# Optimization experiments

Measured on AMD Instinct MI355X. Metric: run time of the kernel, lower is better.

The kernel has to match this reference:

```python
import jax, jax.numpy as jnp
import numpy as np

S = 512      # seq_len -> S*S - S edges
V = 32000    # vocab_size
D = 128      # d_model
H = 4        # num_heads
L = 2        # num_layers
DN = 64      # d_node
DE = 64      # d_edge
DF = 4 * D   # ffn hidden
TEMP = 1.0   # temperature_init
E = S * S - S


def setup_inputs() -> dict:
    key = jax.random.key(0)
    ks = jax.random.split(key, 12)
    n = lambda k, shp: jax.random.normal(k, shp, dtype=jnp.float32) * 0.02
    return {
        "token_ids": jax.random.randint(ks[0], (S,), 0, V),
        "u": jax.random.uniform(ks[1], (E,), dtype=jnp.float32),
        "emb": n(ks[2], (V, D)),
        "Wqkv": n(ks[3], (L, D, 3 * D)), "bqkv": jnp.zeros((L, 3 * D)),
        "Wo": n(ks[4], (L, D, D)), "bo": jnp.zeros((L, D)),
        "ln1_g": jnp.ones((L, D)), "ln1_b": jnp.zeros((L, D)),
        "Wff1": n(ks[5], (L, D, DF)), "bff1": jnp.zeros((L, DF)),
        "Wff2": n(ks[6], (L, DF, D)), "bff2": jnp.zeros((L, D)),
        "ln2_g": jnp.ones((L, D)), "ln2_b": jnp.zeros((L, D)),
        "node_W": n(ks[7], (D, DN)), "node_b": jnp.zeros((DN,)),
        "sc_W1": n(ks[8], (2 * D + 1, D)), "sc_b1": jnp.zeros((D,)),
        "sc_W2": n(ks[9], (D, 1)), "sc_b2": jnp.zeros((1,)),
        "te_W": n(ks[10], (2 * D + 1, DE)), "te_b": jnp.zeros((DE,)),
    }


def _layernorm(x, g, b):
    m = jnp.mean(x, -1, keepdims=True)
    v = jnp.var(x, -1, keepdims=True)
    return (x - m) * jax.lax.rsqrt(v + 1e-5) * g + b


def _pos_encoding(s, d):
    pos = jnp.arange(s, dtype=jnp.float32)[:, None]
    div = jnp.exp(jnp.arange(0, d, 2, dtype=jnp.float32) * (-np.log(10000.0) / d))
    pe = jnp.zeros((s, d), dtype=jnp.float32)
    pe = pe.at[:, 0::2].set(jnp.sin(pos * div)).at[:, 1::2].set(jnp.cos(pos * div))
    return pe


_SRC_NP = np.repeat(np.arange(S), S)
_TGT_NP = np.tile(np.arange(S), S)
_KEEP = _SRC_NP != _TGT_NP
SRC = jnp.asarray(_SRC_NP[_KEEP])  # [E] static off-diagonal indices
TGT = jnp.asarray(_TGT_NP[_KEEP])


def _forward(token_ids, u, emb, Wqkv, bqkv, Wo, bo, ln1_g, ln1_b, Wff1, bff1,
             Wff2, bff2, ln2_g, ln2_b, node_W, node_b, sc_W1, sc_b1, sc_W2,
             sc_b2, te_W, te_b):
    # --- mini transformer backbone ---
    x = emb[token_ids] + _pos_encoding(S, D)  # [S, D]
    dh = D // H
    for l in range(L):
        qkv = x @ Wqkv[l] + bqkv[l]
        q, k, v = jnp.split(qkv, 3, axis=-1)
        q = q.reshape(S, H, dh); k = k.reshape(S, H, dh); v = v.reshape(S, H, dh)
        scores = jnp.einsum('qhd,khd->hqk', q, k) / np.sqrt(dh).astype(np.float32)
        attn = jax.nn.softmax(scores, axis=-1)
        o = jnp.einsum('hqk,khd->qhd', attn, v).reshape(S, D)
        x = _layernorm(x + o @ Wo[l] + bo[l], ln1_g[l], ln1_b[l])
        h = jax.nn.gelu(x @ Wff1[l] + bff1[l], approximate=False)
        x = _layernorm(x + h @ Wff2[l] + bff2[l], ln2_g[l], ln2_b[l])
    node_features = x @ node_W + node_b  # [S, DN]
    # --- all-pairs edge construction (off-diagonal) ---
    pos_diff = ((SRC - TGT).astype(jnp.float32) / S)[:, None]  # [E, 1]
    pair = jnp.concatenate([x[SRC], x[TGT], pos_diff], axis=-1)  # [E, 2D+1]
    # edge scorer MLP
    hs = jax.nn.gelu(pair @ sc_W1 + sc_b1, approximate=False)
    edge_logits = (hs @ sc_W2 + sc_b2)[:, 0]  # [E]
    # gumbel-sigmoid (soft, hard=False)
    uu = jnp.clip(u, 1e-8, 1.0 - 1e-8)
    gnoise = -jnp.log(-jnp.log(uu))
    edge_gates = jax.nn.sigmoid((edge_logits + gnoise) / TEMP)  # [E]
    # gated edge features
    edge_feats = (pair @ te_W + te_b) * edge_gates[:, None]  # [E, DE]
    return node_features, edge_feats, edge_gates


def reference(token_ids, u, emb, Wqkv, bqkv, Wo, bo, ln1_g, ln1_b, Wff1, bff1,
              Wff2, bff2, ln2_g, ln2_b, node_W, node_b, sc_W1, sc_b1, sc_W2,
              sc_b2, te_W, te_b):
    node_features, edge_feats, edge_gates = _forward(
        token_ids, u, emb, Wqkv, bqkv, Wo, bo, ln1_g, ln1_b, Wff1, bff1,
        Wff2, bff2, ln2_g, ln2_b, node_W, node_b, sc_W1, sc_b1, sc_W2,
        sc_b2, te_W, te_b)
    edge_index = jnp.stack([SRC, TGT])  # [2, E]
    return node_features, edge_feats, edge_index, edge_gates
```

## Files before the change

kernel.cpp:

```cpp
#include <hip/hip_runtime.h>
#include <math.h>

#define SS 512
#define DD 128
#define HH 4
#define DHH 32
#define DFF 512
#define E_EDGES 261632

__device__ __forceinline__ float gelu_f(float v) {
    return 0.5f * v * (1.0f + erff(v * 0.70710678118654752f));
}
__device__ __forceinline__ float fgelu(float x) {
    float x2 = x * x;
    float z = x * fmaf(0.044715f, x2, 1.0f) * -1.5957691216057308f;
    float e = __expf(z);
    return x * __builtin_amdgcn_rcpf(1.0f + e);
}

__global__ __launch_bounds__(128) void k_embed(const int* __restrict__ tok,
                                               const float* __restrict__ emb,
                                               float* __restrict__ x) {
    int s = blockIdx.x;
    int d = threadIdx.x;
    float v = emb[(size_t)tok[s] * DD + d];
    int i2 = (d >> 1) << 1;
    float div = expf(-(float)i2 * (9.210340371976184f / 128.0f));
    float arg = (float)s * div;
    v += (d & 1) ? cosf(arg) : sinf(arg);
    x[s * DD + d] = v;
}

__global__ __launch_bounds__(384) void k_qkv(const float* __restrict__ x,
                                             const float* __restrict__ W,
                                             const float* __restrict__ b,
                                             float* __restrict__ qkv) {
    __shared__ float xs[4][DD];
    int r0 = blockIdx.x * 4;
    int c = threadIdx.x;
    for (int i = threadIdx.x; i < 4 * DD; i += 384)
        xs[i >> 7][i & 127] = x[(r0 + (i >> 7)) * DD + (i & 127)];
    __syncthreads();
    float a0 = 0, a1 = 0, a2 = 0, a3 = 0;
    for (int d = 0; d < DD; ++d) {
        float w = W[d * 384 + c];
        a0 += xs[0][d] * w; a1 += xs[1][d] * w;
        a2 += xs[2][d] * w; a3 += xs[3][d] * w;
    }
    float bb = b[c];
    qkv[(r0 + 0) * 384 + c] = a0 + bb;
    qkv[(r0 + 1) * 384 + c] = a1 + bb;
    qkv[(r0 + 2) * 384 + c] = a2 + bb;
    qkv[(r0 + 3) * 384 + c] = a3 + bb;
}

__global__ __launch_bounds__(256) void k_attn(const float* __restrict__ qkv,
                                              float* __restrict__ o) {
    int qi = blockIdx.x;
    int tid = threadIdx.x;
    int h = tid >> 6, lane = tid & 63;
    __shared__ float sq[DD];
    __shared__ float ps[HH][SS];
    __shared__ float tile[64 * 129];
    if (tid < DD) sq[tid] = qkv[qi * 384 + tid];
    const float scale = 0.17677669529663687f;
    float sc[8];
    float m = -1e30f;
    for (int kk = 0; kk < 8; ++kk) {
        __syncthreads();
        for (int i = tid * 4; i < 64 * 128; i += 1024) {
            int r = i >> 7, c = i & 127;
            const float4 v = *reinterpret_cast<const float4*>(&qkv[(kk * 64 + r) * 384 + 128 + c]);
            tile[r * 129 + c + 0] = v.x;
            tile[r * 129 + c + 1] = v.y;
            tile[r * 129 + c + 2] = v.z;
            tile[r * 129 + c + 3] = v.w;
        }
        __syncthreads();
        float acc = 0.f;
        #pragma unroll
        for (int d = 0; d < DHH; ++d)
            acc += sq[h * DHH + d] * tile[lane * 129 + h * DHH + d];
        acc *= scale;
        sc[kk] = acc;
        m = fmaxf(m, acc);
    }
    for (int off = 32; off; off >>= 1) m = fmaxf(m, __shfl_xor(m, off));
    float sum = 0.f;
    for (int kk = 0; kk < 8; ++kk) { sc[kk] = __expf(sc[kk] - m); sum += sc[kk]; }
    for (int off = 32; off; off >>= 1) sum += __shfl_xor(sum, off);
    float inv = 1.0f / sum;
    for (int kk = 0; kk < 8; ++kk) ps[h][kk * 64 + lane] = sc[kk] * inv;
    __syncthreads();
    int d = lane & 31, hh2 = lane >> 5;
    float acc = 0.f;
    for (int i = 0; i < 256; ++i) {
        int ki = hh2 * 256 + i;
        acc += ps[h][ki] * qkv[ki * 384 + 256 + h * DHH + d];
    }
    acc += __shfl_down(acc, 32);
    if (lane < 32) o[qi * DD + h * DHH + d] = acc;
}

__global__ __launch_bounds__(256) void k_tail(const float* __restrict__ o,
                                              const float* __restrict__ Wo,
                                              const float* __restrict__ bo,
                                              const float* __restrict__ g1,
                                              const float* __restrict__ b1,
                                              const float* __restrict__ W1,
                                              const float* __restrict__ bf1,
                                              const float* __restrict__ W2,
                                              const float* __restrict__ bf2,
                                              const float* __restrict__ g2,
                                              const float* __restrict__ b2,
                                              float* __restrict__ x) {
    int r0 = blockIdx.x * 2;
    int tid = threadIdx.x;
    int grp = tid >> 7, c = tid & 127;
    int wig = (tid >> 6) & 1;
    __shared__ float osr[2][DD];
    __shared__ float x1[2][DD];
    __shared__ float hh[2][DFF];
    __shared__ float red[2][2];
    osr[grp][c] = o[(r0 + grp) * DD + c];
    float xres = x[(r0 + grp) * DD + c];
    __syncthreads();
    float acc = 0.f;
    for (int d = 0; d < DD; ++d) acc += osr[grp][d] * Wo[d * DD + c];
    float val = xres + acc + bo[c];
    float sum = val;
    for (int off = 32; off; off >>= 1) sum += __shfl_xor(sum, off);
    if ((tid & 63) == 0) red[grp][wig] = sum;
    __syncthreads();
    float mean = (red[grp][0] + red[grp][1]) * (1.0f / 128.0f);
    float dv = val - mean;
    float sq = dv * dv;
    for (int off = 32; off; off >>= 1) sq += __shfl_xor(sq, off);
    __syncthreads();
    if ((tid & 63) == 0) red[grp][wig] = sq;
    __syncthreads();
    float var = (red[grp][0] + red[grp][1]) * (1.0f / 128.0f);
    float xv = dv * rsqrtf(var + 1e-5f) * g1[c] + b1[c];
    x1[grp][c] = xv;
    __syncthreads();
    {
        int c0 = tid, c1 = tid + 256;
        float s00 = 0, s01 = 0, s10 = 0, s11 = 0;
        for (int d = 0; d < DD; ++d) {
            float xa = x1[0][d], xb = x1[1][d];
            float w0 = W1[d * DFF + c0], w1 = W1[d * DFF + c1];
            s00 = fmaf(xa, w0, s00); s10 = fmaf(xb, w0, s10);
            s01 = fmaf(xa, w1, s01); s11 = fmaf(xb, w1, s11);
        }
        hh[0][c0] = gelu_f(s00 + bf1[c0]);
        hh[1][c0] = gelu_f(s10 + bf1[c0]);
        hh[0][c1] = gelu_f(s01 + bf1[c1]);
        hh[1][c1] = gelu_f(s11 + bf1[c1]);
    }
    __syncthreads();
    float acc2 = 0.f;
    for (int d = 0; d < DFF; ++d) acc2 += hh[grp][d] * W2[d * DD + c];
    float val2 = x1[grp][c] + acc2 + bf2[c];
    float sum2 = val2;
    for (int off = 32; off; off >>= 1) sum2 += __shfl_xor(sum2, off);
    if ((tid & 63) == 0) red[grp][wig] = sum2;
    __syncthreads();
    float mean2 = (red[grp][0] + red[grp][1]) * (1.0f / 128.0f);
    float dv2 = val2 - mean2;
    float sq2 = dv2 * dv2;
    for (int off = 32; off; off >>= 1) sq2 += __shfl_xor(sq2, off);
    __syncthreads();
    if ((tid & 63) == 0) red[grp][wig] = sq2;
    __syncthreads();
    float var2 = (red[grp][0] + red[grp][1]) * (1.0f / 128.0f);
    x[(r0 + grp) * DD + c] = dv2 * rsqrtf(var2 + 1e-5f) * g2[c] + b2[c];
}

__global__ __launch_bounds__(448) void k_node_pre(const float* __restrict__ x,
                                                  const float* __restrict__ nodeW,
                                                  const float* __restrict__ nodeb,
                                                  const float* __restrict__ scW1,
                                                  const float* __restrict__ scb1,
                                                  const float* __restrict__ teW,
                                                  const float* __restrict__ teb,
                                                  float* __restrict__ out_node,
                                                  float* __restrict__ As,
                                                  float* __restrict__ At2,
                                                  float* __restrict__ Bs,
                                                  float* __restrict__ Bt) {
    __shared__ float xs[4][DD];
    int r0 = blockIdx.x * 4;
    for (int i = threadIdx.x; i < 4 * DD; i += 448)
        xs[i >> 7][i & 127] = x[(r0 + (i >> 7)) * DD + (i & 127)];
    __syncthreads();
    int c = threadIdx.x;
    const float* wp;
    int ldw;
    if (c < 64)       { wp = nodeW + c;                    ldw = 64;  }
    else if (c < 192) { wp = scW1 + (c - 64);              ldw = 128; }
    else if (c < 320) { wp = scW1 + 128 * 128 + (c - 192); ldw = 128; }
    else if (c < 384) { wp = teW + (c - 320);              ldw = 64;  }
    else              { wp = teW + 128 * 64 + (c - 384);   ldw = 64;  }
    float a[4] = {0, 0, 0, 0};
    for (int d = 0; d < DD; ++d) {
        float w = wp[d * ldw];
        a[0] += xs[0][d] * w; a[1] += xs[1][d] * w;
        a[2] += xs[2][d] * w; a[3] += xs[3][d] * w;
    }
    #pragma unroll
    for (int r = 0; r < 4; ++r) {
        int row = r0 + r;
        float v = a[r];
        if (c < 64)       out_node[row * 64 + c] = v + nodeb[c];
        else if (c < 192) As[row * 128 + (c - 64)] = v + scb1[c - 64];
        else if (c < 320) {
            int j = c - 192;
            At2[row * 128 + ((j & 63) * 2 + (j >> 6))] = v;
        }
        else if (c < 384) Bs[row * 64 + (c - 320)] = v + teb[c - 320];
        else              Bt[row * 64 + (c - 384)] = v;
    }
}

__global__ __launch_bounds__(256) void k_estatic(const float* __restrict__ u,
                                                 float* __restrict__ nl,
                                                 float* __restrict__ out_ei) {
    int e = blockIdx.x * 256 + threadIdx.x;
    if (e >= E_EDGES) return;
    int s = e / 511;
    int idx = e - s * 511;
    int t = idx + (idx >= s);
    out_ei[e] = (float)s;
    out_ei[E_EDGES + e] = (float)t;
    float uu = fminf(fmaxf(u[e], 1e-8f), 1.0f - 1e-8f);
    nl[e] = -__logf(uu);
}

__global__ __launch_bounds__(256) void k_edges(const float* __restrict__ As,
                                               const float* __restrict__ At2,
                                               const float* __restrict__ Bs,
                                               const float* __restrict__ Bt,
                                               const float* __restrict__ scW1,
                                               const float* __restrict__ scW2,
                                               const float* __restrict__ scb2p,
                                               const float* __restrict__ teW,
                                               const float* __restrict__ nl,
                                               float* __restrict__ out_feat,
                                               float* __restrict__ out_gate) {
    int s = blockIdx.x;
    int seg = blockIdx.y;
    __shared__ float lAs[128], lap[128], lw2[128], lBs[64], lbp[64];
    int tid = threadIdx.x;
    if (tid < 128) {
        lAs[tid] = As[s * 128 + tid];
        lap[tid] = scW1[256 * 128 + tid];
        lw2[tid] = scW2[tid];
    } else if (tid < 192) {
        int j = tid - 128;
        lBs[j] = Bs[s * 64 + j];
        lbp[j] = teW[256 * 64 + j];
    }
    __syncthreads();
    float scb2 = scb2p[0];
    int w = tid >> 6, lane = tid & 63;
    int j = lane;
    float cAs0 = lAs[j], cAs1 = lAs[j + 64];
    float cap0 = lap[j], cap1 = lap[j + 64];
    float cw0 = lw2[j], cw1 = lw2[j + 64];
    float cBs = lBs[j], cbp = lbp[j];
    for (int iter = 0; iter < 16; ++iter) {
        int idx = seg * 64 + iter * 4 + w;
        if (idx >= 511) continue;
        int t = idx + (idx >= s);
        int e = s * 511 + idx;
        float pd = (float)(s - t) * (1.0f / 512.0f);
        float2 at = *reinterpret_cast<const float2*>(&At2[(size_t)t * 128 + 2 * j]);
        float a0 = cAs0 + at.x + pd * cap0;
        float a1 = cAs1 + at.y + pd * cap1;
        float part = fgelu(a0) * cw0 + fgelu(a1) * cw1;
        for (int off = 32; off; off >>= 1) part += __shfl_xor(part, off);
        float logit = part + scb2;
        float gate = __builtin_amdgcn_rcpf(1.0f + nl[e] * __expf(-logit));
        float f = (cBs + Bt[t * 64 + j] + pd * cbp) * gate;
        out_feat[(size_t)e * 64 + j] = f;
        if (lane == 0) out_gate[e] = gate;
    }
}

extern "C" void kernel_launch(void* const* d_in, const int* in_sizes, int n_in,
                              void* d_out, int out_size, void* d_ws, size_t ws_size,
                              hipStream_t stream) {
    const int*   tok   = (const int*)d_in[0];
    const float* u     = (const float*)d_in[1];
    const float* emb   = (const float*)d_in[2];
    const float* Wqkv  = (const float*)d_in[3];
    const float* bqkv  = (const float*)d_in[4];
    const float* Wo    = (const float*)d_in[5];
    const float* bo    = (const float*)d_in[6];
    const float* ln1g  = (const float*)d_in[7];
    const float* ln1b  = (const float*)d_in[8];
    const float* Wff1  = (const float*)d_in[9];
    const float* bff1  = (const float*)d_in[10];
    const float* Wff2  = (const float*)d_in[11];
    const float* bff2  = (const float*)d_in[12];
    const float* ln2g  = (const float*)d_in[13];
    const float* ln2b  = (const float*)d_in[14];
    const float* nodeW = (const float*)d_in[15];
    const float* nodeb = (const float*)d_in[16];
    const float* scW1  = (const float*)d_in[17];
    const float* scb1  = (const float*)d_in[18];
    const float* scW2  = (const float*)d_in[19];
    const float* scb2  = (const float*)d_in[20];
    const float* teW   = (const float*)d_in[21];
    const float* teb   = (const float*)d_in[22];

    float* out      = (float*)d_out;
    float* out_node = out;
    float* out_feat = out + 512 * 64;
    float* out_ei   = out_feat + (size_t)E_EDGES * 64;
    float* out_gate = out_ei + 2 * (size_t)E_EDGES;

    float* ws   = (float*)d_ws;
    float* x    = ws;
    float* qkv  = x + 512 * 128;
    float* o    = qkv + 512 * 384;
    float* As   = o + 512 * 128;
    float* At2  = As + 512 * 128;
    float* Bs   = At2 + 512 * 128;
    float* Bt   = Bs + 512 * 64;
    float* nl   = Bt + 512 * 64;

    k_estatic<<<dim3((E_EDGES + 255) / 256), dim3(256), 0, stream>>>(u, nl, out_ei);
    k_embed<<<dim3(512), dim3(128), 0, stream>>>(tok, emb, x);
    for (int l = 0; l < 2; ++l) {
        k_qkv<<<dim3(128), dim3(384), 0, stream>>>(x, Wqkv + l * 128 * 384, bqkv + l * 384, qkv);
        k_attn<<<dim3(512), dim3(256), 0, stream>>>(qkv, o);
        k_tail<<<dim3(256), dim3(256), 0, stream>>>(o, Wo + l * 128 * 128, bo + l * 128,
                                                    ln1g + l * 128, ln1b + l * 128,
                                                    Wff1 + l * 128 * 512, bff1 + l * 512,
                                                    Wff2 + l * 512 * 128, bff2 + l * 128,
                                                    ln2g + l * 128, ln2b + l * 128, x);
    }
    k_node_pre<<<dim3(128), dim3(448), 0, stream>>>(x, nodeW, nodeb, scW1, scb1, teW, teb,
                                                    out_node, As, At2, Bs, Bt);
    k_edges<<<dim3(512, 8), dim3(256), 0, stream>>>(As, At2, Bs, Bt, scW1, scW2, scb2, teW, nl,
                                                    out_feat, out_gate);
}
```

Before: 287.7 us.

## Fuse prologue kernels, pair queries in attention, repack edge data for vector loads

Merges the edge-static and embedding kernels into one launch. Halves the rows per QKV block so more blocks run, and has each attention block handle two queries so the staged K tile is reused. Repacks At and Bt so each edge kernel thread loads float4 vectors and handles 8 hidden units, with the gelu reduction done across 16 lanes and 4 edges per wavefront. The edge grid shrinks to match the new per-block coverage, and gelu constants are folded. Output stores become strided by 16, which may reduce coalescing.

New measurement: 277.7 us. -3.5%, faster.

```diff
diff --git a/kernel.cpp b/kernel.cpp
--- a/kernel.cpp
+++ b/kernel.cpp
@@ -13,59 +13,74 @@
 }
 __device__ __forceinline__ float fgelu(float x) {
     float x2 = x * x;
-    float z = x * fmaf(0.044715f, x2, 1.0f) * -1.5957691216057308f;
+    float z = x * fmaf(-0.0713548164f, x2, -1.5957691216f);
     float e = __expf(z);
     return x * __builtin_amdgcn_rcpf(1.0f + e);
 }
 
-__global__ __launch_bounds__(128) void k_embed(const int* __restrict__ tok,
-                                               const float* __restrict__ emb,
-                                               float* __restrict__ x) {
-    int s = blockIdx.x;
-    int d = threadIdx.x;
-    float v = emb[(size_t)tok[s] * DD + d];
-    int i2 = (d >> 1) << 1;
-    float div = expf(-(float)i2 * (9.210340371976184f / 128.0f));
-    float arg = (float)s * div;
-    v += (d & 1) ? cosf(arg) : sinf(arg);
-    x[s * DD + d] = v;
+__global__ __launch_bounds__(256) void k_pre(const float* __restrict__ u,
+                                             float* __restrict__ nl,
+                                             float* __restrict__ out_ei,
+                                             const int* __restrict__ tok,
+                                             const float* __restrict__ emb,
+                                             float* __restrict__ x) {
+    int b = blockIdx.x;
+    if (b < 1022) {
+        int e = b * 256 + threadIdx.x;
+        if (e >= E_EDGES) return;
+        int s = e / 511;
+        int idx = e - s * 511;
+        int t = idx + (idx >= s);
+        out_ei[e] = (float)s;
+        out_ei[E_EDGES + e] = (float)t;
+        float uu = fminf(fmaxf(u[e], 1e-8f), 1.0f - 1e-8f);
+        nl[e] = -__logf(uu);
+    } else {
+        int i = (b - 1022) * 256 + threadIdx.x;
+        int s = i >> 7, d = i & 127;
+        float v = emb[(size_t)tok[s] * DD + d];
+        int i2 = (d >> 1) << 1;
+        float div = expf(-(float)i2 * (9.210340371976184f / 128.0f));
+        float arg = (float)s * div;
+        v += (d & 1) ? cosf(arg) : sinf(arg);
+        x[i] = v;
+    }
 }
 
 __global__ __launch_bounds__(384) void k_qkv(const float* __restrict__ x,
                                              const float* __restrict__ W,
                                              const float* __restrict__ b,
                                              float* __restrict__ qkv) {
-    __shared__ float xs[4][DD];
-    int r0 = blockIdx.x * 4;
+    __shared__ float xs[2][DD];
+    int r0 = blockIdx.x * 2;
     int c = threadIdx.x;
-    for (int i = threadIdx.x; i < 4 * DD; i += 384)
-        xs[i >> 7][i & 127] = x[(r0 + (i >> 7)) * DD + (i & 127)];
-    __syncthreads();
-    float a0 = 0, a1 = 0, a2 = 0, a3 = 0;
+    if (c < 256) xs[c >> 7][c & 127] = x[r0 * DD + c];
+    __syncthreads();
+    float a0 = 0, a1 = 0;
     for (int d = 0; d < DD; ++d) {
         float w = W[d * 384 + c];
         a0 += xs[0][d] * w; a1 += xs[1][d] * w;
-        a2 += xs[2][d] * w; a3 += xs[3][d] * w;
     }
     float bb = b[c];
     qkv[(r0 + 0) * 384 + c] = a0 + bb;
     qkv[(r0 + 1) * 384 + c] = a1 + bb;
-    qkv[(r0 + 2) * 384 + c] = a2 + bb;
-    qkv[(r0 + 3) * 384 + c] = a3 + bb;
 }
 
 __global__ __launch_bounds__(256) void k_attn(const float* __restrict__ qkv,
                                               float* __restrict__ o) {
-    int qi = blockIdx.x;
+    int q0 = blockIdx.x * 2, q1 = q0 + 1;
     int tid = threadIdx.x;
     int h = tid >> 6, lane = tid & 63;
-    __shared__ float sq[DD];
-    __shared__ float ps[HH][SS];
+    __shared__ float sq[2][DD];
+    __shared__ float ps[2][HH][SS];
     __shared__ float tile[64 * 129];
-    if (tid < DD) sq[tid] = qkv[qi * 384 + tid];
+    if (tid < 128) {
+        sq[0][tid] = qkv[q0 * 384 + tid];
+        sq[1][tid] = qkv[q1 * 384 + tid];
+    }
     const float scale = 0.17677669529663687f;
-    float sc[8];
-    float m = -1e30f;
+    float sc0[8], sc1[8];
+    float m0 = -1e30f, m1 = -1e30f;
     for (int kk = 0; kk < 8; ++kk) {
         __syncthreads();
         for (int i = tid * 4; i < 64 * 128; i += 1024) {
@@ -77,29 +92,49 @@
             tile[r * 129 + c + 3] = v.w;
         }
         __syncthreads();
-        float acc = 0.f;
+        float a0 = 0.f, a1 = 0.f;
         #pragma unroll
-        for (int d = 0; d < DHH; ++d)
-            acc += sq[h * DHH + d] * tile[lane * 129 + h * DHH + d];
-        acc *= scale;
-        sc[kk] = acc;
-        m = fmaxf(m, acc);
-    }
-    for (int off = 32; off; off >>= 1) m = fmaxf(m, __shfl_xor(m, off));
-    float sum = 0.f;
-    for (int kk = 0; kk < 8; ++kk) { sc[kk] = __expf(sc[kk] - m); sum += sc[kk]; }
-    for (int off = 32; off; off >>= 1) sum += __shfl_xor(sum, off);
-    float inv = 1.0f / sum;
-    for (int kk = 0; kk < 8; ++kk) ps[h][kk * 64 + lane] = sc[kk] * inv;
+        for (int d = 0; d < DHH; ++d) {
+            float kv = tile[lane * 129 + h * DHH + d];
+            a0 += sq[0][h * DHH + d] * kv;
+            a1 += sq[1][h * DHH + d] * kv;
+        }
+        sc0[kk] = a0 * scale; sc1[kk] = a1 * scale;
+        m0 = fmaxf(m0, sc0[kk]); m1 = fmaxf(m1, sc1[kk]);
+    }
+    for (int off = 32; off; off >>= 1) {
+        m0 = fmaxf(m0, __shfl_xor(m0, off));
+        m1 = fmaxf(m1, __shfl_xor(m1, off));
+    }
+    float s0 = 0.f, s1 = 0.f;
+    for (int kk = 0; kk < 8; ++kk) {
+        sc0[kk] = __expf(sc0[kk] - m0); s0 += sc0[kk];
+        sc1[kk] = __expf(sc1[kk] - m1); s1 += sc1[kk];
+    }
+    for (int off = 32; off; off >>= 1) {
+        s0 += __shfl_xor(s0, off);
+        s1 += __shfl_xor(s1, off);
+    }
+    float i0 = 1.0f / s0, i1 = 1.0f / s1;
+    for (int kk = 0; kk < 8; ++kk) {
+        ps[0][h][kk * 64 + lane] = sc0[kk] * i0;
+        ps[1][h][kk * 64 + lane] = sc1[kk] * i1;
+    }
     __syncthreads();
     int d = lane & 31, hh2 = lane >> 5;
-    float acc = 0.f;
+    float a0 = 0.f, a1 = 0.f;
     for (int i = 0; i < 256; ++i) {
         int ki = hh2 * 256 + i;
-        acc += ps[h][ki] * qkv[ki * 384 + 256 + h * DHH + d];
-    }
-    acc += __shfl_down(acc, 32);
-    if (lane < 32) o[qi * DD + h * DHH + d] = acc;
+        float v = qkv[ki * 384 + 256 + h * DHH + d];
+        a0 += ps[0][h][ki] * v;
+        a1 += ps[1][h][ki] * v;
+    }
+    a0 += __shfl_down(a0, 32);
+    a1 += __shfl_down(a1, 32);
+    if (lane < 32) {
+        o[q0 * DD + h * DHH + d] = a0;
+        o[q1 * DD + h * DHH + d] = a1;
+    }
 }
 
 __global__ __launch_bounds__(256) void k_tail(const float* __restrict__ o,
@@ -185,9 +220,9 @@
                                                   const float* __restrict__ teb,
                                                   float* __restrict__ out_node,
                                                   float* __restrict__ As,
-                                                  float* __restrict__ At2,
+                                                  float* __restrict__ Atp,
                                                   float* __restrict__ Bs,
-                                                  float* __restrict__ Bt) {
+                                                  float* __restrict__ Btp) {
     __shared__ float xs[4][DD];
     int r0 = blockIdx.x * 4;
     for (int i = threadIdx.x; i < 4 * DD; i += 448)
@@ -214,32 +249,24 @@
         if (c < 64)       out_node[row * 64 + c] = v + nodeb[c];
         else if (c < 192) As[row * 128 + (c - 64)] = v + scb1[c - 64];
         else if (c < 320) {
-            int j = c - 192;
-            At2[row * 128 + ((j & 63) * 2 + (j >> 6))] = v;
+            int j0 = c - 192;
+            int hhi = j0 >> 6, rem = j0 & 63;
+            int jj = rem & 15, k = rem >> 4;
+            Atp[row * 128 + jj * 8 + k * 2 + hhi] = v;
         }
         else if (c < 384) Bs[row * 64 + (c - 320)] = v + teb[c - 320];
-        else              Bt[row * 64 + (c - 384)] = v;
-    }
-}
-
-__global__ __launch_bounds__(256) void k_estatic(const float* __restrict__ u,
-                                                 float* __restrict__ nl,
-                                                 float* __restrict__ out_ei) {
-    int e = blockIdx.x * 256 + threadIdx.x;
-    if (e >= E_EDGES) return;
-    int s = e / 511;
-    int idx = e - s * 511;
-    int t = idx + (idx >= s);
-    out_ei[e] = (float)s;
-    out_ei[E_EDGES + e] = (float)t;
-    float uu = fminf(fmaxf(u[e], 1e-8f), 1.0f - 1e-8f);
-    nl[e] = -__logf(uu);
+        else {
+            int jf = c - 384;
+            int jj = jf & 15, k = jf >> 4;
+            Btp[row * 64 + jj * 4 + k] = v;
+        }
+    }
 }
 
 __global__ __launch_bounds__(256) void k_edges(const float* __restrict__ As,
-                                               const float* __restrict__ At2,
+                                               const float* __restrict__ Atp,
                                                const float* __restrict__ Bs,
-                                               const float* __restrict__ Bt,
+                                               const float* __restrict__ Btp,
                                                const float* __restrict__ scW1,
                                                const float* __restrict__ scW2,
                                                const float* __restrict__ scb2p,
@@ -261,29 +288,54 @@
         lbp[j] = teW[256 * 64 + j];
     }
     __syncthreads();
+    int w = tid >> 6, lane = tid & 63;
+    int g = lane >> 4, jj = lane & 15;
+    float rAs[8], rap[8], rw2[8], rBs[4], rbp[4];
+    #pragma unroll
+    for (int k = 0; k < 4; ++k) {
+        int j = jj + 16 * k;
+        rAs[2 * k] = lAs[j]; rAs[2 * k + 1] = lAs[j + 64];
+        rap[2 * k] = lap[j]; rap[2 * k + 1] = lap[j + 64];
+        rw2[2 * k] = lw2[j]; rw2[2 * k + 1] = lw2[j + 64];
+        rBs[k] = lBs[j]; rbp[k] = lbp[j];
+    }
     float scb2 = scb2p[0];
-    int w = tid >> 6, lane = tid & 63;
-    int j = lane;
-    float cAs0 = lAs[j], cAs1 = lAs[j + 64];
-    float cap0 = lap[j], cap1 = lap[j + 64];
-    float cw0 = lw2[j], cw1 = lw2[j + 64];
-    float cBs = lBs[j], cbp = lbp[j];
     for (int iter = 0; iter < 16; ++iter) {
-        int idx = seg * 64 + iter * 4 + w;
+        int idx = seg * 256 + w * 64 + iter * 4 + g;
         if (idx >= 511) continue;
         int t = idx + (idx >= s);
         int e = s * 511 + idx;
         float pd = (float)(s - t) * (1.0f / 512.0f);
-        float2 at = *reinterpret_cast<const float2*>(&At2[(size_t)t * 128 + 2 * j]);
-        float a0 = cAs0 + at.x + pd * cap0;
-        float a1 = cAs1 + at.y + pd * cap1;
-        float part = fgelu(a0) * cw0 + fgelu(a1) * cw1;
-        for (int off = 32; off; off >>= 1) part += __shfl_xor(part, off);
+        const float4* ap = reinterpret_cast<const float4*>(&Atp[(size_t)t * 128 + jj * 8]);
+        float4 at0 = ap[0];
+        float4 at1 = ap[1];
+        float part;
+        float a;
+        a = fmaf(pd, rap[0], rAs[0] + at0.x); part  = fgelu(a) * rw2[0];
+        a = fmaf(pd, rap[1], rAs[1] + at0.y); part += fgelu(a) * rw2[1];
+        a = fmaf(pd, rap[2], rAs[2] + at0.z); part += fgelu(a) * rw2[2];
+        a = fmaf(pd, rap[3], rAs[3] + at0.w); part += fgelu(a) * rw2[3];
+        a = fmaf(pd, rap[4], rAs[4] + at1.x); part += fgelu(a) * rw2[4];
+        a = fmaf(pd, rap[5], rAs[5] + at1.y); part += fgelu(a) * rw2[5];
+        a = fmaf(pd, rap[6], rAs[6] + at1.z); part += fgelu(a) * rw2[6];
+        a = fmaf(pd, rap[7], rAs[7] + at1.w); part += fgelu(a) * rw2[7];
+        part += __shfl_xor(part, 1);
+        part += __shfl_xor(part, 2);
+        part += __shfl_xor(part, 4);
+        part += __shfl_xor(part, 8);
         float logit = part + scb2;
         float gate = __builtin_amdgcn_rcpf(1.0f + nl[e] * __expf(-logit));
-        float f = (cBs + Bt[t * 64 + j] + pd * cbp) * gate;
-        out_feat[(size_t)e * 64 + j] = f;
-        if (lane == 0) out_gate[e] = gate;
+        float4 bt = *reinterpret_cast<const float4*>(&Btp[(size_t)t * 64 + jj * 4]);
+        float f0 = fmaf(pd, rbp[0], rBs[0] + bt.x) * gate;
+        float f1 = fmaf(pd, rbp[1], rBs[1] + bt.y) * gate;
+        float f2 = fmaf(pd, rbp[2], rBs[2] + bt.z) * gate;
+        float f3 = fmaf(pd, rbp[3], rBs[3] + bt.w) * gate;
+        size_t base = (size_t)e * 64 + jj;
+        out_feat[base + 0]  = f0;
+        out_feat[base + 16] = f1;
+        out_feat[base + 32] = f2;
+        out_feat[base + 48] = f3;
+        if (jj == 0) out_gate[e] = gate;
     }
 }
 
@@ -325,16 +377,15 @@
     float* qkv  = x + 512 * 128;
     float* o    = qkv + 512 * 384;
     float* As   = o + 512 * 128;
-    float* At2  = As + 512 * 128;
-    float* Bs   = At2 + 512 * 128;
-    float* Bt   = Bs + 512 * 64;
-    float* nl   = Bt + 512 * 64;
-
-    k_estatic<<<dim3((E_EDGES + 255) / 256), dim3(256), 0, stream>>>(u, nl, out_ei);
-    k_embed<<<dim3(512), dim3(128), 0, stream>>>(tok, emb, x);
+    float* Atp  = As + 512 * 128;
+    float* Bs   = Atp + 512 * 128;
+    float* Btp  = Bs + 512 * 64;
+    float* nl   = Btp + 512 * 64;
+
+    k_pre<<<dim3(1278), dim3(256), 0, stream>>>(u, nl, out_ei, tok, emb, x);
     for (int l = 0; l < 2; ++l) {
-        k_qkv<<<dim3(128), dim3(384), 0, stream>>>(x, Wqkv + l * 128 * 384, bqkv + l * 384, qkv);
-        k_attn<<<dim3(512), dim3(256), 0, stream>>>(qkv, o);
+        k_qkv<<<dim3(256), dim3(384), 0, stream>>>(x, Wqkv + l * 128 * 384, bqkv + l * 384, qkv);
+        k_attn<<<dim3(256), dim3(256), 0, stream>>>(qkv, o);
         k_tail<<<dim3(256), dim3(256), 0, stream>>>(o, Wo + l * 128 * 128, bo + l * 128,
                                                     ln1g + l * 128, ln1b + l * 128,
                                                     Wff1 + l * 128 * 512, bff1 + l * 512,
@@ -342,7 +393,7 @@
                                                     ln2g + l * 128, ln2b + l * 128, x);
     }
     k_node_pre<<<dim3(128), dim3(448), 0, stream>>>(x, nodeW, nodeb, scW1, scb1, teW, teb,
-                                                    out_node, As, At2, Bs, Bt);
-    k_edges<<<dim3(512, 8), dim3(256), 0, stream>>>(As, At2, Bs, Bt, scW1, scW2, scb2, teW, nl,
+                                                    out_node, As, Atp, Bs, Btp);
+    k_edges<<<dim3(512, 2), dim3(256), 0, stream>>>(As, Atp, Bs, Btp, scW1, scW2, scb2, teW, nl,
                                                     out_feat, out_gate);
 }
```
